# Kernel tuning notes

Hardware: AMD Instinct MI355X
Metric: run time of the kernel (lower is better)

The kernel has to match this reference:

```python
import jax, jax.numpy as jnp
import numpy as np

NUM_HEADS = 4
NUM_POINTS = 8


def deform_attn_3d(q, value, ref, Hf, Wf, Wv, bv, Wo, bo, Wa, ba):
    # q: (BS,N,C)  value: (BS,Hf*Wf,C)  ref: (BS,N,D,2) normalized (x,y) in [0,1]
    BS, N, C = q.shape
    H, P = NUM_HEADS, NUM_POINTS
    D = ref.shape[2]
    c = C // H
    # value projection, split heads: (BS,H,M,c)
    v = (value @ Wv + bv).reshape(BS, Hf * Wf, H, c).transpose(0, 2, 1, 3)
    # sampling offsets and attention weights from the query
    off = (q @ Wo + bo).reshape(BS, N, H, P, 2)
    attn = jax.nn.softmax((q @ Wa + ba).reshape(BS, N, H, P), axis=-1)
    # normalize offsets by (W,H); distribute P points over D z-anchors (P//D per anchor)
    norm = jnp.array([Wf, Hf], dtype=q.dtype)
    off = off.reshape(BS, N, H, P // D, D, 2) / norm
    loc = (ref[:, :, None, None, :, :] + off).reshape(BS, N, H, P, 2)
    # grid_sample(align_corners=False, padding=zeros): pixel = loc*size - 0.5
    x = loc[..., 0] * Wf - 0.5
    y = loc[..., 1] * Hf - 0.5
    x0f = jnp.floor(x)
    y0f = jnp.floor(y)
    lx = x - x0f
    ly = y - y0f
    x0 = x0f.astype(jnp.int32)
    y0 = y0f.astype(jnp.int32)

    def tohead(a):  # (BS,N,H,P) -> (BS,H,N*P)
        return a.transpose(0, 2, 1, 3).reshape(BS, H, N * P)

    def gather(yy, xx):
        valid = ((xx >= 0) & (xx < Wf) & (yy >= 0) & (yy < Hf)).astype(q.dtype)
        idx = jnp.clip(yy, 0, Hf - 1) * Wf + jnp.clip(xx, 0, Wf - 1)
        g = jnp.take_along_axis(v, tohead(idx)[..., None], axis=2)  # (BS,H,N*P,c)
        return g * tohead(valid)[..., None]

    out = (gather(y0, x0) * tohead((1 - lx) * (1 - ly))[..., None]
           + gather(y0, x0 + 1) * tohead(lx * (1 - ly))[..., None]
           + gather(y0 + 1, x0) * tohead((1 - lx) * ly)[..., None]
           + gather(y0 + 1, x0 + 1) * tohead(lx * ly)[..., None])
    out = (out * tohead(attn)[..., None]).reshape(BS, H, N, P, c).sum(3)  # (BS,H,N,c)
    return out.transpose(0, 2, 1, 3).reshape(BS, N, C)


def spatial_cross_attention(query, query_pos, value, reference_points_cam, bev_mask,
                            Hf, Wf, Wv, bv, Wo, bo, Wa, ba, Wout, bout):
    # query/query_pos: (B,N,C); value: (S,M,B,C); ref: (S,B,N,D,2); bev_mask: (S,B,N,D)
    B, N, C = query.shape
    S, M = value.shape[0], value.shape[1]
    D = reference_points_cam.shape[3]
    q = query + query_pos
    # broadcast queries over cameras (mask-equivalent of the torch rebatch/compaction):
    # deformable attention is per-query independent, so computing all queries per cam
    # and masking invalid ones is the same math as rebatch+scatter.
    q_all = jnp.broadcast_to(q[:, None], (B, S, N, C)).reshape(B * S, N, C)
    v_all = value.transpose(2, 0, 1, 3).reshape(B * S, M, C)
    ref = reference_points_cam.transpose(1, 0, 2, 3, 4).reshape(B * S, N, D, 2)
    out = deform_attn_3d(q_all, v_all, ref, Hf, Wf, Wv, bv, Wo, bo, Wa, ba)
    out = out.reshape(B, S, N, C)
    mask_q = (bev_mask.sum(-1) > 0).astype(query.dtype)  # (S,B,N): query hits this cam
    slots = (out * mask_q.transpose(1, 0, 2)[..., None]).sum(1)  # (B,N,C)
    count = jnp.maximum(mask_q.sum(0), 1.0)  # (B,N) clamp(min=1)
    slots = slots / count[..., None]
    # output_proj, dropout (eval -> identity), residual with original query
    return slots @ Wout + bout + query


def setup_inputs() -> dict:
    B, S, N, Z, C = 1, 6, 16384, 8, 128
    Hf, Wf = 28, 50
    H, P = NUM_HEADS, NUM_POINTS
    rng = jax.random.key(0)
    ks = jax.random.split(rng, 12)
    return {
        "query": jax.random.normal(ks[0], (B, N, C), jnp.float32),
        "query_pos": 0.1 * jax.random.normal(ks[1], (B, N, C), jnp.float32),
        "value": jax.random.normal(ks[2], (S, Hf * Wf, B, C), jnp.float32),
        "reference_points_cam": jax.random.uniform(ks[3], (S, B, N, Z, 2), jnp.float32),
        "bev_mask": jax.random.randint(ks[4], (S, B, N, Z), 0, 2).astype(bool),
        "Wv": 0.02 * jax.random.normal(ks[5], (C, C), jnp.float32),
        "bv": jnp.zeros((C,), jnp.float32),
        "Wo": 0.02 * jax.random.normal(ks[6], (C, H * P * 2), jnp.float32),
        "bo": 0.5 * jax.random.normal(ks[7], (H * P * 2,), jnp.float32),
        "Wa": 0.02 * jax.random.normal(ks[8], (C, H * P), jnp.float32),
        "ba": jnp.zeros((H * P,), jnp.float32),
        "Wout": 0.02 * jax.random.normal(ks[9], (C, C), jnp.float32),
        "bout": jnp.zeros((C,), jnp.float32),
        "Hf": Hf,
        "Wf": Wf,
    }


def reference(query, query_pos, value, reference_points_cam, bev_mask,
              Wv, bv, Wo, bo, Wa, ba, Wout, bout, Hf, Wf):
    return spatial_cross_attention(query, query_pos, value, reference_points_cam, bev_mask,
                                   Hf, Wf, Wv, bv, Wo, bo, Wa, ba, Wout, bout)
```

## Files before the change

kernel.cpp:

```cpp
#include <hip/hip_runtime.h>

#define N_Q   16384
#define C_DIM 128
#define S_CAM 6
#define M_VAL 1400
#define D_Z   8
#define HF    28
#define WF    50
#define QPB   8

__device__ __forceinline__ float bflo(unsigned u){ return __uint_as_float(u << 16); }
__device__ __forceinline__ float bfhi(unsigned u){ return __uint_as_float(u & 0xffff0000u); }

__device__ __forceinline__ bool mask_any(const unsigned char* __restrict__ mask,
                                         int mflag, size_t mbase){
  if(mflag==0){
    int any=0;
    #pragma unroll
    for(int d=0;d<D_Z;d++) any |= mask[mbase+d];
    return any!=0;
  } else if(mflag==1){
    const int* mp = (const int*)mask;  int any=0;
    #pragma unroll
    for(int d=0;d<D_Z;d++) any |= mp[mbase+d];
    return any!=0;
  } else {
    const long long* mp = (const long long*)mask;  long long any=0;
    #pragma unroll
    for(int d=0;d<D_Z;d++) any |= mp[mbase+d];
    return any!=0;
  }
}

__global__ __launch_bounds__(256)
void value_proj_kernel(const float* __restrict__ value,
                       const float* __restrict__ Wv,
                       const float* __restrict__ bv,
                       unsigned short* __restrict__ vb16,
                       const unsigned char* __restrict__ mask,
                       int* __restrict__ flag){
  __shared__ float tile[8][C_DIM];
  __shared__ int s_cntA, s_cntB;
  const int tid = threadIdx.x;
  const int col = tid & 127;
  const int rh  = tid >> 7;
  const int r0  = blockIdx.x * 8;
  if(blockIdx.x==0 && tid==0){ s_cntA=0; s_cntB=0; }
  {
    const float4* src = (const float4*)(value + (size_t)r0*C_DIM);
    ((float4*)&tile[0][0])[tid] = src[tid];
  }
  __syncthreads();
  float acc[4];
  const float bias = bv[col];
  #pragma unroll
  for(int r=0;r<4;r++) acc[r]=bias;
  for(int k=0;k<C_DIM;k+=4){
    const float w0 = Wv[(k+0)*C_DIM + col];
    const float w1 = Wv[(k+1)*C_DIM + col];
    const float w2 = Wv[(k+2)*C_DIM + col];
    const float w3 = Wv[(k+3)*C_DIM + col];
    #pragma unroll
    for(int r=0;r<4;r++){
      const float4 t = *(const float4*)&tile[rh*4+r][k];
      acc[r] += t.x*w0 + t.y*w1 + t.z*w2 + t.w*w3;
    }
  }
  #pragma unroll
  for(int r=0;r<4;r++){
    unsigned u = __float_as_uint(acc[r]);
    u += 0x7fff + ((u >> 16) & 1);
    vb16[(size_t)(r0+rh*4+r)*C_DIM + col] = (unsigned short)(u >> 16);
  }
  if(blockIdx.x==0){
    int a=0, b=0;
    for(int i=tid;i<1024;i+=256){
      const unsigned char v = mask[i];
      if(((i&3)!=0) && v) a=1;
      if(((i&7)==4) && v) b=1;
    }
    if(a) atomicOr(&s_cntA,1);
    if(b) atomicOr(&s_cntB,1);
    __syncthreads();
    if(tid==0) flag[0] = s_cntA ? 0 : (s_cntB ? 1 : 2);
  }
}

__global__ __launch_bounds__(256, 4)
void fused_deform_kernel(const unsigned short* __restrict__ vb16,
                         const float* __restrict__ query,
                         const float* __restrict__ query_pos,
                         const float* __restrict__ Wo, const float* __restrict__ bo,
                         const float* __restrict__ Wa, const float* __restrict__ ba,
                         const float* __restrict__ ref,
                         const unsigned char* __restrict__ mask,
                         const int* __restrict__ flag,
                         const float* __restrict__ Wout,
                         const float* __restrict__ bout,
                         float* __restrict__ out){
  __shared__ float  qs[QPB][C_DIM+4];
  __shared__ float  offs[QPB][68];
  __shared__ float  attns[QPB][36];
  __shared__ float  logits[QPB][36];
  __shared__ float2 refs[QPB][S_CAM*D_Z];
  __shared__ int    activ[QPB][S_CAM];
  __shared__ float  cinv[QPB];

  const int tid = threadIdx.x;
  const int n0  = blockIdx.x * QPB;
  const int mflag = flag[0];
  const int qi = tid >> 5;
  const int l  = tid & 31;

  const int e1 = tid;
  const int e2 = tid + 256;
  const int q1 = e1/48, r1 = e1%48;
  float2 ra = ((const float2*)ref)[((size_t)(r1>>3)*N_Q + (n0+q1))*D_Z + (r1&7)];
  float2 rb = make_float2(0.f,0.f);
  if(e2 < QPB*S_CAM*D_Z){
    const int q2 = e2/48, r2i = e2%48;
    rb = ((const float2*)ref)[((size_t)(r2i>>3)*N_Q + (n0+q2))*D_Z + (r2i&7)];
  }

  {
    const float4* qa = (const float4*)(query     + (size_t)n0*C_DIM);
    const float4* qb = (const float4*)(query_pos + (size_t)n0*C_DIM);
    const int r = tid >> 5, c4 = tid & 31;
    float4 A = qa[tid], B = qb[tid];
    *(float4*)&qs[r][c4*4] = make_float4(A.x+B.x, A.y+B.y, A.z+B.z, A.w+B.w);
  }
  __syncthreads();

  {
    float acc0 = bo[l], acc1 = bo[l+32], acc2 = ba[l];
    for(int k=0;k<C_DIM;k++){
      const float qv = qs[qi][k];
      acc0 += qv * Wo[k*64 + l];
      acc1 += qv * Wo[k*64 + l + 32];
      acc2 += qv * Wa[k*32 + l];
    }
    offs[qi][l]    = acc0;
    offs[qi][l+32] = acc1;
    logits[qi][l]  = acc2;
  }
  refs[q1][r1] = ra;
  if(e2 < QPB*S_CAM*D_Z) refs[e2/48][e2%48] = rb;
  if(tid < QPB*S_CAM){
    const int q2 = tid / S_CAM, s = tid % S_CAM;
    activ[q2][s] = mask_any(mask, mflag, ((size_t)s*N_Q + (n0+q2))*D_Z) ? 1 : 0;
  }
  __syncthreads();
  if(tid < 32){
    const int q2 = tid >> 2, h = tid & 3;
    const float* L = &logits[q2][h*8];
    float mx = L[0];
    #pragma unroll
    for(int p=1;p<8;p++) mx = fmaxf(mx, L[p]);
    float e[8], ssum = 0.f;
    #pragma unroll
    for(int p=0;p<8;p++){ e[p] = __expf(L[p]-mx); ssum += e[p]; }
    const float inv = 1.f/ssum;
    #pragma unroll
    for(int p=0;p<8;p++) attns[q2][h*8+p] = e[p]*inv;
  } else if(tid >= 256-QPB){
    const int q2 = tid - (256-QPB);
    int c = 0;
    #pragma unroll
    for(int s=0;s<S_CAM;s++) c += activ[q2][s];
    cinv[q2] = 1.f / fmaxf((float)c, 1.f);
  }
  __syncthreads();

  const int gh  = l >> 3;
  const int gch = gh*32 + (l&7)*4;
  float ax=0.f, ay=0.f, az=0.f, aw=0.f;

  for(int s=0;s<S_CAM;s++){
    if(!activ[qi][s]) continue;
    const unsigned short* vb = vb16 + (size_t)s*M_VAL*C_DIM + gch;
    #pragma unroll
    for(int p=0;p<8;p++){
      const float2 r2 = refs[qi][s*8+p];
      const float ox = offs[qi][gh*16+p*2+0];
      const float oy = offs[qi][gh*16+p*2+1];
      const float x = fmaf(r2.x, (float)WF, ox - 0.5f);
      const float y = fmaf(r2.y, (float)HF, oy - 0.5f);
      const float x0f = floorf(x), y0f = floorf(y);
      const float fx = x - x0f,    fy = y - y0f;
      const int x0 = (int)x0f, y0 = (int)y0f;
      const int x1 = x0+1,     y1 = y0+1;
      const float at = attns[qi][gh*8+p];
      const float wx0 = (x0>=0 && x0<WF) ? (1.f-fx) : 0.f;
      const float wx1 = (x1>=0 && x1<WF) ? fx       : 0.f;
      const float wy0 = ((y0>=0 && y0<HF) ? (1.f-fy) : 0.f) * at;
      const float wy1 = ((y1>=0 && y1<HF) ? fy       : 0.f) * at;
      const int x0c = min(max(x0,0), WF-1), x1c = min(max(x1,0), WF-1);
      const int y0c = min(max(y0,0), HF-1), y1c = min(max(y1,0), HF-1);
      const float w00 = wx0*wy0, w01 = wx1*wy0, w10 = wx0*wy1, w11 = wx1*wy1;
      const uint2 a0 = *(const uint2*)(vb + (y0c*WF+x0c)*C_DIM);
      const uint2 a1 = *(const uint2*)(vb + (y0c*WF+x1c)*C_DIM);
      const uint2 a2 = *(const uint2*)(vb + (y1c*WF+x0c)*C_DIM);
      const uint2 a3 = *(const uint2*)(vb + (y1c*WF+x1c)*C_DIM);
      ax += w00*bflo(a0.x) + w01*bflo(a1.x) + w10*bflo(a2.x) + w11*bflo(a3.x);
      ay += w00*bfhi(a0.x) + w01*bfhi(a1.x) + w10*bfhi(a2.x) + w11*bfhi(a3.x);
      az += w00*bflo(a0.y) + w01*bflo(a1.y) + w10*bflo(a2.y) + w11*bflo(a3.y);
      aw += w00*bfhi(a0.y) + w01*bfhi(a1.y) + w10*bfhi(a2.y) + w11*bfhi(a3.y);
    }
  }

  __syncthreads();
  {
    const float inv = cinv[qi];
    *(float4*)&qs[qi][gch] = make_float4(ax*inv, ay*inv, az*inv, aw*inv);
  }
  __syncthreads();
  {
    const int c4 = l;
    const int n  = n0 + qi;
    const float4 b4 = *(const float4*)&bout[c4*4];
    const float4 r4 = *(const float4*)&query[(size_t)n*C_DIM + c4*4];
    float ox = b4.x + r4.x, oy = b4.y + r4.y, oz = b4.z + r4.z, ow = b4.w + r4.w;
    for(int k=0;k<C_DIM;k++){
      const float sv = qs[qi][k];
      const float4 w = *(const float4*)&Wout[(size_t)k*C_DIM + c4*4];
      ox += sv*w.x; oy += sv*w.y; oz += sv*w.z; ow += sv*w.w;
    }
    *(float4*)&out[(size_t)n*C_DIM + c4*4] = make_float4(ox, oy, oz, ow);
  }
}

extern "C" void kernel_launch(void* const* d_in, const int* in_sizes, int n_in,
                              void* d_out, int out_size, void* d_ws, size_t ws_size,
                              hipStream_t stream){
  const float* query     = (const float*)d_in[0];
  const float* query_pos = (const float*)d_in[1];
  const float* value     = (const float*)d_in[2];
  const float* ref       = (const float*)d_in[3];
  const unsigned char* mask = (const unsigned char*)d_in[4];
  const float* Wv   = (const float*)d_in[5];
  const float* bv   = (const float*)d_in[6];
  const float* Wo   = (const float*)d_in[7];
  const float* bo   = (const float*)d_in[8];
  const float* Wa   = (const float*)d_in[9];
  const float* ba   = (const float*)d_in[10];
  const float* Wout = (const float*)d_in[11];
  const float* bout = (const float*)d_in[12];
  float* out = (float*)d_out;

  int* flag = (int*)d_ws;
  unsigned short* vb16 = (unsigned short*)((char*)d_ws + 64);

  value_proj_kernel<<<(S_CAM*M_VAL)/8, 256, 0, stream>>>(value, Wv, bv, vb16, mask, flag);
  fused_deform_kernel<<<N_Q/QPB, 256, 0, stream>>>(vb16, query, query_pos,
                                                   Wo, bo, Wa, ba, ref, mask, flag,
                                                   Wout, bout, out);
}
```

Before: 204.7 us.

## Process 16 queries per block with 8 channels per thread in fused kernel

Doubles the queries handled per 256-thread block by halving lanes per query. Each thread now covers 8 channels, using 16-byte bf16 gathers for the bilinear corners and 8-wide accumulators in the offset/attention and output projections. The aim is fewer, wider memory transactions and more reuse of each weight load per thread. The cost is higher register pressure and fewer blocks in the grid, which may lower occupancy under the 256x4 launch bound.

```diff
diff --git a/kernel.cpp b/kernel.cpp
--- a/kernel.cpp
+++ b/kernel.cpp
@@ -7,7 +7,7 @@
 #define D_Z   8
 #define HF    28
 #define WF    50
-#define QPB   8
+#define QPB   16
 
 __device__ __forceinline__ float bflo(unsigned u){ return __uint_as_float(u << 16); }
 __device__ __forceinline__ float bfhi(unsigned u){ return __uint_as_float(u & 0xffff0000u); }
@@ -102,55 +102,62 @@
   __shared__ float  offs[QPB][68];
   __shared__ float  attns[QPB][36];
   __shared__ float  logits[QPB][36];
-  __shared__ float2 refs[QPB][S_CAM*D_Z];
+  __shared__ float2 refs[QPB][S_CAM*D_Z+1];
   __shared__ int    activ[QPB][S_CAM];
   __shared__ float  cinv[QPB];
 
   const int tid = threadIdx.x;
   const int n0  = blockIdx.x * QPB;
   const int mflag = flag[0];
-  const int qi = tid >> 5;
-  const int l  = tid & 31;
-
-  const int e1 = tid;
-  const int e2 = tid + 256;
-  const int q1 = e1/48, r1 = e1%48;
-  float2 ra = ((const float2*)ref)[((size_t)(r1>>3)*N_Q + (n0+q1))*D_Z + (r1&7)];
-  float2 rb = make_float2(0.f,0.f);
-  if(e2 < QPB*S_CAM*D_Z){
-    const int q2 = e2/48, r2i = e2%48;
-    rb = ((const float2*)ref)[((size_t)(r2i>>3)*N_Q + (n0+q2))*D_Z + (r2i&7)];
+  const int qi = tid >> 4;
+  const int l  = tid & 15;
+
+  float2 rpre[3];
+  #pragma unroll
+  for(int j=0;j<3;j++){
+    const int e = tid + 256*j;
+    const int q = e/48, r = e%48;
+    rpre[j] = ((const float2*)ref)[((size_t)(r>>3)*N_Q + (n0+q))*D_Z + (r&7)];
   }
 
   {
     const float4* qa = (const float4*)(query     + (size_t)n0*C_DIM);
     const float4* qb = (const float4*)(query_pos + (size_t)n0*C_DIM);
-    const int r = tid >> 5, c4 = tid & 31;
-    float4 A = qa[tid], B = qb[tid];
-    *(float4*)&qs[r][c4*4] = make_float4(A.x+B.x, A.y+B.y, A.z+B.z, A.w+B.w);
-  }
-  __syncthreads();
-
-  {
-    float acc0 = bo[l], acc1 = bo[l+32], acc2 = ba[l];
+    #pragma unroll
+    for(int j=0;j<2;j++){
+      const int idx = tid + 256*j;
+      const int r = idx >> 5, c4 = idx & 31;
+      float4 A = qa[idx], B = qb[idx];
+      *(float4*)&qs[r][c4*4] = make_float4(A.x+B.x, A.y+B.y, A.z+B.z, A.w+B.w);
+    }
+  }
+  __syncthreads();
+
+  {
+    float ao0 = bo[l*4+0], ao1 = bo[l*4+1], ao2 = bo[l*4+2], ao3 = bo[l*4+3];
+    float aa0 = ba[l*2+0], aa1 = ba[l*2+1];
     for(int k=0;k<C_DIM;k++){
       const float qv = qs[qi][k];
-      acc0 += qv * Wo[k*64 + l];
-      acc1 += qv * Wo[k*64 + l + 32];
-      acc2 += qv * Wa[k*32 + l];
-    }
-    offs[qi][l]    = acc0;
-    offs[qi][l+32] = acc1;
-    logits[qi][l]  = acc2;
-  }
-  refs[q1][r1] = ra;
-  if(e2 < QPB*S_CAM*D_Z) refs[e2/48][e2%48] = rb;
+      const float4 wo = *(const float4*)&Wo[k*64 + l*4];
+      const float2 wa = *(const float2*)&Wa[k*32 + l*2];
+      ao0 += qv*wo.x; ao1 += qv*wo.y; ao2 += qv*wo.z; ao3 += qv*wo.w;
+      aa0 += qv*wa.x; aa1 += qv*wa.y;
+    }
+    offs[qi][l*4+0] = ao0;  offs[qi][l*4+1] = ao1;
+    offs[qi][l*4+2] = ao2;  offs[qi][l*4+3] = ao3;
+    logits[qi][l*2+0] = aa0;  logits[qi][l*2+1] = aa1;
+  }
+  #pragma unroll
+  for(int j=0;j<3;j++){
+    const int e = tid + 256*j;
+    refs[e/48][e%48] = rpre[j];
+  }
   if(tid < QPB*S_CAM){
     const int q2 = tid / S_CAM, s = tid % S_CAM;
     activ[q2][s] = mask_any(mask, mflag, ((size_t)s*N_Q + (n0+q2))*D_Z) ? 1 : 0;
   }
   __syncthreads();
-  if(tid < 32){
+  if(tid < 64){
     const int q2 = tid >> 2, h = tid & 3;
     const float* L = &logits[q2][h*8];
     float mx = L[0];
@@ -171,9 +178,9 @@
   }
   __syncthreads();
 
-  const int gh  = l >> 3;
-  const int gch = gh*32 + (l&7)*4;
-  float ax=0.f, ay=0.f, az=0.f, aw=0.f;
+  const int gh  = l >> 2;
+  const int gch = gh*32 + (l&3)*8;
+  float a0=0.f,a1=0.f,a2=0.f,a3=0.f,a4=0.f,a5=0.f,a6=0.f,a7=0.f;
 
   for(int s=0;s<S_CAM;s++){
     if(!activ[qi][s]) continue;
@@ -197,35 +204,46 @@
       const int x0c = min(max(x0,0), WF-1), x1c = min(max(x1,0), WF-1);
       const int y0c = min(max(y0,0), HF-1), y1c = min(max(y1,0), HF-1);
       const float w00 = wx0*wy0, w01 = wx1*wy0, w10 = wx0*wy1, w11 = wx1*wy1;
-      const uint2 a0 = *(const uint2*)(vb + (y0c*WF+x0c)*C_DIM);
-      const uint2 a1 = *(const uint2*)(vb + (y0c*WF+x1c)*C_DIM);
-      const uint2 a2 = *(const uint2*)(vb + (y1c*WF+x0c)*C_DIM);
-      const uint2 a3 = *(const uint2*)(vb + (y1c*WF+x1c)*C_DIM);
-      ax += w00*bflo(a0.x) + w01*bflo(a1.x) + w10*bflo(a2.x) + w11*bflo(a3.x);
-      ay += w00*bfhi(a0.x) + w01*bfhi(a1.x) + w10*bfhi(a2.x) + w11*bfhi(a3.x);
-      az += w00*bflo(a0.y) + w01*bflo(a1.y) + w10*bflo(a2.y) + w11*bflo(a3.y);
-      aw += w00*bfhi(a0.y) + w01*bfhi(a1.y) + w10*bfhi(a2.y) + w11*bfhi(a3.y);
+      const uint4 v00 = *(const uint4*)(vb + (y0c*WF+x0c)*C_DIM);
+      const uint4 v01 = *(const uint4*)(vb + (y0c*WF+x1c)*C_DIM);
+      const uint4 v10 = *(const uint4*)(vb + (y1c*WF+x0c)*C_DIM);
+      const uint4 v11 = *(const uint4*)(vb + (y1c*WF+x1c)*C_DIM);
+      a0 += w00*bflo(v00.x) + w01*bflo(v01.x) + w10*bflo(v10.x) + w11*bflo(v11.x);
+      a1 += w00*bfhi(v00.x) + w01*bfhi(v01.x) + w10*bfhi(v10.x) + w11*bfhi(v11.x);
+      a2 += w00*bflo(v00.y) + w01*bflo(v01.y) + w10*bflo(v10.y) + w11*bflo(v11.y);
+      a3 += w00*bfhi(v00.y) + w01*bfhi(v01.y) + w10*bfhi(v10.y) + w11*bfhi(v11.y);
+      a4 += w00*bflo(v00.z) + w01*bflo(v01.z) + w10*bflo(v10.z) + w11*bflo(v11.z);
+      a5 += w00*bfhi(v00.z) + w01*bfhi(v01.z) + w10*bfhi(v10.z) + w11*bfhi(v11.z);
+      a6 += w00*bflo(v00.w) + w01*bflo(v01.w) + w10*bflo(v10.w) + w11*bflo(v11.w);
+      a7 += w00*bfhi(v00.w) + w01*bfhi(v01.w) + w10*bfhi(v10.w) + w11*bfhi(v11.w);
     }
   }
 
   __syncthreads();
   {
     const float inv = cinv[qi];
-    *(float4*)&qs[qi][gch] = make_float4(ax*inv, ay*inv, az*inv, aw*inv);
-  }
-  __syncthreads();
-  {
-    const int c4 = l;
+    *(float4*)&qs[qi][gch]   = make_float4(a0*inv, a1*inv, a2*inv, a3*inv);
+    *(float4*)&qs[qi][gch+4] = make_float4(a4*inv, a5*inv, a6*inv, a7*inv);
+  }
+  __syncthreads();
+  {
+    const int c0 = l*8;
     const int n  = n0 + qi;
-    const float4 b4 = *(const float4*)&bout[c4*4];
-    const float4 r4 = *(const float4*)&query[(size_t)n*C_DIM + c4*4];
-    float ox = b4.x + r4.x, oy = b4.y + r4.y, oz = b4.z + r4.z, ow = b4.w + r4.w;
+    const float4 bA = *(const float4*)&bout[c0];
+    const float4 bB = *(const float4*)&bout[c0+4];
+    const float4 rA = *(const float4*)&query[(size_t)n*C_DIM + c0];
+    const float4 rB = *(const float4*)&query[(size_t)n*C_DIM + c0 + 4];
+    float o0=bA.x+rA.x, o1=bA.y+rA.y, o2=bA.z+rA.z, o3=bA.w+rA.w;
+    float o4=bB.x+rB.x, o5=bB.y+rB.y, o6=bB.z+rB.z, o7=bB.w+rB.w;
     for(int k=0;k<C_DIM;k++){
       const float sv = qs[qi][k];
-      const float4 w = *(const float4*)&Wout[(size_t)k*C_DIM + c4*4];
-      ox += sv*w.x; oy += sv*w.y; oz += sv*w.z; ow += sv*w.w;
-    }
-    *(float4*)&out[(size_t)n*C_DIM + c4*4] = make_float4(ox, oy, oz, ow);
+      const float4 wA = *(const float4*)&Wout[(size_t)k*C_DIM + c0];
+      const float4 wB = *(const float4*)&Wout[(size_t)k*C_DIM + c0 + 4];
+      o0 += sv*wA.x; o1 += sv*wA.y; o2 += sv*wA.z; o3 += sv*wA.w;
+      o4 += sv*wB.x; o5 += sv*wB.y; o6 += sv*wB.z; o7 += sv*wB.w;
+    }
+    *(float4*)&out[(size_t)n*C_DIM + c0]     = make_float4(o0,o1,o2,o3);
+    *(float4*)&out[(size_t)n*C_DIM + c0 + 4] = make_float4(o4,o5,o6,o7);
   }
 }
 
```

Measured after the change: 519.4 us. 2.54x slower.
